# Kernel optimization log

Hardware: AMD Instinct MI355X
Metric: run time of the kernel (lower is better)

The kernel has to match this reference:

```python
import jax, jax.numpy as jnp
import numpy as np

NODE_CARDS = [119, 5, 12, 12, 10, 6, 6, 2, 2]
EDGE_CARDS = [5, 6, 2]
HIDDEN = 256
LAYERS = 5
N = 60000
E = 180000
G = 2048  # num graphs (fixed num_segments)
BN_EPS = 1e-5

_NODE_OFFS = np.concatenate([[0], np.cumsum(NODE_CARDS[:-1])]).astype(np.int32)
_EDGE_OFFS = np.concatenate([[0], np.cumsum(EDGE_CARDS[:-1])]).astype(np.int32)
_NODE_MAX = np.asarray(NODE_CARDS, np.int32) - 1
_EDGE_MAX = np.asarray(EDGE_CARDS, np.int32) - 1


def _cat_sum(x, table, maxs, offs):
    # x: [N, F] int; table: [sum(cards), H] -> [N, H]
    idx = jnp.clip(x, 0, maxs[None, :]) + offs[None, :]
    return table[idx].sum(axis=1)


def setup_inputs() -> dict:
    key = jax.random.key(0)
    ks = jax.random.split(key, 32)
    w = 0.0625  # ~ xavier for 256

    def nrm(k, shape, s=w):
        return jax.random.normal(k, shape, dtype=jnp.float32) * s

    inp = {
        'x': jax.random.randint(ks[0], (N, len(NODE_CARDS)), 0, 119, dtype=jnp.int32),
        'edge_index': jax.random.randint(ks[1], (2, E), 0, N, dtype=jnp.int32),
        'edge_attr': jax.random.randint(ks[2], (E, len(EDGE_CARDS)), 0, 6, dtype=jnp.int32),
        'batch': jnp.sort(jax.random.randint(ks[3], (N,), 0, G, dtype=jnp.int32)),
        # embeddings
        'node_emb': nrm(ks[4], (int(sum(NODE_CARDS)), HIDDEN), 0.1),
        'edge_emb': nrm(ks[5], (int(sum(EDGE_CARDS)), HIDDEN), 0.1),
        'vn_emb': nrm(ks[6], (1, HIDDEN), 0.1),
        # GINE conv: eps + 2-layer MLP per layer (stacked)
        'eps': jnp.zeros((LAYERS,), jnp.float32),
        'W1': nrm(ks[7], (LAYERS, HIDDEN, HIDDEN)),
        'b1': jnp.zeros((LAYERS, HIDDEN), jnp.float32),
        'W2': nrm(ks[8], (LAYERS, HIDDEN, HIDDEN)),
        'b2': jnp.zeros((LAYERS, HIDDEN), jnp.float32),
        # BatchNorm (eval mode: running stats)
        'bn_gamma': jnp.ones((LAYERS, HIDDEN), jnp.float32),
        'bn_beta': jnp.zeros((LAYERS, HIDDEN), jnp.float32),
        'bn_mean': nrm(ks[9], (LAYERS, HIDDEN), 0.02),
        'bn_var': jnp.ones((LAYERS, HIDDEN), jnp.float32),
        # virtual-node MLP per layer
        'vW1': nrm(ks[10], (LAYERS, HIDDEN, HIDDEN)),
        'vb1': jnp.zeros((LAYERS, HIDDEN), jnp.float32),
        'vW2': nrm(ks[11], (LAYERS, HIDDEN, HIDDEN)),
        'vb2': jnp.zeros((LAYERS, HIDDEN), jnp.float32),
        # head MLP (2 layers: hidden->hidden->1)
        'hW1': nrm(ks[12], (HIDDEN, HIDDEN)),
        'hb1': jnp.zeros((HIDDEN,), jnp.float32),
        'hW2': nrm(ks[13], (HIDDEN, 1)),
        'hb2': jnp.zeros((1,), jnp.float32),
    }
    return inp


def reference(x, edge_index, edge_attr, batch,
              node_emb, edge_emb, vn_emb, eps,
              W1, b1, W2, b2,
              bn_gamma, bn_beta, bn_mean, bn_var,
              vW1, vb1, vW2, vb2,
              hW1, hb1, hW2, hb2):
    node_maxs = jnp.asarray(_NODE_MAX)
    node_offs = jnp.asarray(_NODE_OFFS)
    edge_maxs = jnp.asarray(_EDGE_MAX)
    edge_offs = jnp.asarray(_EDGE_OFFS)

    h = _cat_sum(x, node_emb, node_maxs, node_offs)          # [N, H]
    ea = _cat_sum(edge_attr, edge_emb, edge_maxs, edge_offs)  # [E, H]
    src, dst = edge_index[0], edge_index[1]

    vn = jnp.broadcast_to(vn_emb[0], (G, HIDDEN))  # [G, H]

    def mean_pool(h_):
        s = jax.ops.segment_sum(h_, batch, num_segments=G)
        cnt = jax.ops.segment_sum(jnp.ones((h_.shape[0], 1), h_.dtype), batch, num_segments=G)
        return s / jnp.maximum(cnt, 1.0)

    for l in range(LAYERS):
        h = h + vn[batch]
        # GINEConv: msg = relu(x_src + edge_attr); agg scatter-add onto dst
        msg = jax.nn.relu(h[src] + ea)                        # [E, H]
        agg = jax.ops.segment_sum(msg, dst, num_segments=N)   # [N, H]
        z = (1.0 + eps[l]) * h + agg
        z = jax.nn.relu(z @ W1[l] + b1[l]) @ W2[l] + b2[l]
        # BatchNorm1d (eval, running stats)
        z = (z - bn_mean[l]) * (bn_gamma[l] / jnp.sqrt(bn_var[l] + BN_EPS)) + bn_beta[l]
        h = jax.nn.relu(z)
        # virtual-node update
        g = mean_pool(h)
        vn = vn + (jax.nn.relu(g @ vW1[l] + vb1[l]) @ vW2[l] + vb2[l])

    g = mean_pool(h)                                          # [G, H]
    logits = (jax.nn.relu(g @ hW1 + hb1) @ hW2 + hb2).reshape(-1)  # [G]
    return logits
```

## Files before the change

### kernel.cpp

```cpp
#include <hip/hip_runtime.h>

#define NN 60000
#define NE 180000
#define NG 2048
#define HD 256
#define NL 5
#define CAP 32

typedef unsigned short u16;
typedef unsigned int u32;
typedef __bf16 bf16x8 __attribute__((ext_vector_type(8)));
typedef float f32x4 __attribute__((ext_vector_type(4)));

__device__ __forceinline__ u16 f2bf(float f) {
    u32 u = __builtin_bit_cast(u32, f);
    u += 0x7FFFu + ((u >> 16) & 1u);
    return (u16)(u >> 16);
}
__device__ __forceinline__ float bf2f(u16 s) {
    return __builtin_bit_cast(float, (u32)s << 16);
}
__device__ __forceinline__ void gload_lds16(const void* g, void* l) {
    __builtin_amdgcn_global_load_lds(
        (const __attribute__((address_space(1))) unsigned int*)g,
        (__attribute__((address_space(3))) unsigned int*)l, 16, 0, 0);
}

__constant__ int NODE_OFF[9]  = {0, 119, 124, 136, 148, 158, 164, 170, 172};
__constant__ int NODE_MAXC[9] = {118, 4, 11, 11, 9, 5, 5, 1, 1};

__global__ __launch_bounds__(256) void k_prep_weights(
    const float* __restrict__ W1, const float* __restrict__ W2,
    const float* __restrict__ vW1, const float* __restrict__ vW2,
    const float* __restrict__ hW1, u16* __restrict__ Wt)
{
    int mat = blockIdx.x >> 8;
    int n = blockIdx.x & 255;
    int k = threadIdx.x;
    const float* src;
    if (mat < 5)       src = W1 + (size_t)mat * 65536;
    else if (mat < 10) src = W2 + (size_t)(mat - 5) * 65536;
    else if (mat < 15) src = vW1 + (size_t)(mat - 10) * 65536;
    else if (mat < 20) src = vW2 + (size_t)(mat - 15) * 65536;
    else               src = hW1;
    Wt[(size_t)mat * 65536 + n * 256 + k] = f2bf(src[k * 256 + n]);
}

__global__ __launch_bounds__(256) void k_comb(const float* __restrict__ eemb,
                                              u16* __restrict__ comb)
{
    int r = blockIdx.x;
    int c = threadIdx.x;
    int a0 = r / 12, a1 = (r % 12) / 2, a2 = r & 1;
    comb[r * 256 + c] = f2bf(eemb[(0 + a0) * 256 + c] + eemb[(5 + a1) * 256 + c] +
                             eemb[(11 + a2) * 256 + c]);
}

__global__ __launch_bounds__(256) void k_starts(const int* __restrict__ batch,
                                                int* __restrict__ starts)
{
    int g = blockIdx.x * 256 + threadIdx.x;
    if (g > NG) return;
    int lo = 0, hi = NN;
    while (lo < hi) {
        int mid = (lo + hi) >> 1;
        if (batch[mid] < g) lo = mid + 1; else hi = mid;
    }
    starts[g] = lo;
}

__global__ __launch_bounds__(256) void k_vn_init(const float* __restrict__ vn_emb,
                                                 float* __restrict__ vn,
                                                 u16* __restrict__ vnbf)
{
    int i = blockIdx.x * 256 + threadIdx.x;
    float v = vn_emb[i & 255];
    vn[i] = v;
    vnbf[i] = f2bf(v);
}

__global__ __launch_bounds__(256) void k_embed(const int* __restrict__ x,
                                               const float* __restrict__ node_emb,
                                               u16* __restrict__ hbf)
{
    int i = blockIdx.x * 4 + (threadIdx.x >> 6);
    if (i >= NN) return;
    int c = (threadIdx.x & 63) * 4;
    float4 s = make_float4(0.f, 0.f, 0.f, 0.f);
#pragma unroll
    for (int f = 0; f < 9; ++f) {
        int xv = x[i * 9 + f];
        xv = xv < 0 ? 0 : (xv > NODE_MAXC[f] ? NODE_MAXC[f] : xv);
        const float4 t = *(const float4*)&node_emb[(size_t)(NODE_OFF[f] + xv) * 256 + c];
        s.x += t.x; s.y += t.y; s.z += t.z; s.w += t.w;
    }
    ushort4 o;
    o.x = f2bf(s.x); o.y = f2bf(s.y); o.z = f2bf(s.z); o.w = f2bf(s.w);
    *(ushort4*)&hbf[(size_t)i * 256 + c] = o;
}

__global__ __launch_bounds__(256) void k_bucket(
    const int* __restrict__ src, const int* __restrict__ dst,
    const int* __restrict__ eattr, int* __restrict__ deg, u32* __restrict__ slots)
{
    int e = blockIdx.x * 256 + threadIdx.x;
    if (e >= NE) return;
    int a0 = eattr[e * 3 + 0]; a0 = a0 < 0 ? 0 : (a0 > 4 ? 4 : a0);
    int a1 = eattr[e * 3 + 1]; a1 = a1 < 0 ? 0 : (a1 > 5 ? 5 : a1);
    int a2 = eattr[e * 3 + 2]; a2 = a2 < 0 ? 0 : (a2 > 1 ? 1 : a2);
    u32 code = (u32)(a0 * 12 + a1 * 2 + a2);
    int d = dst[e];
    int p = atomicAdd(&deg[d], 1);
    if (p < CAP) slots[(size_t)d * CAP + p] = (u32)src[e] | (code << 17);
}

__global__ __launch_bounds__(256) void k_agg(
    const u16* __restrict__ hbf, const u16* __restrict__ vnbf,
    const int* __restrict__ batch, const u32* __restrict__ slots,
    const int* __restrict__ deg, const u16* __restrict__ comb,
    u16* __restrict__ Abf, const float* __restrict__ epsp)
{
    int d = blockIdx.x * 4 + (threadIdx.x >> 6);
    int lane = threadIdx.x & 63;
    int c = lane * 4;
    int nd = deg[d];
    nd = nd > CAP ? CAP : nd;

    const u32* sl = slots + (size_t)d * CAP;
    u32 sv_l = (lane < nd) ? sl[lane] : 0u;
    int b_l = (lane < nd) ? batch[sv_l & 0x1FFFFu] : 0;

    float4 acc = make_float4(0.f, 0.f, 0.f, 0.f);
    for (int p = 0; p < nd; ++p) {
        u32 sv = (u32)__shfl((int)sv_l, p);
        int b  = __shfl(b_l, p);
        int s  = (int)(sv & 0x1FFFFu);
        int code = (int)(sv >> 17);
        const ushort4 hv = *(const ushort4*)&hbf[(size_t)s * 256 + c];
        const ushort4 vv = *(const ushort4*)&vnbf[(size_t)b * 256 + c];
        const ushort4 tv = *(const ushort4*)&comb[(size_t)code * 256 + c];
        acc.x += fmaxf(bf2f(hv.x) + bf2f(vv.x) + bf2f(tv.x), 0.f);
        acc.y += fmaxf(bf2f(hv.y) + bf2f(vv.y) + bf2f(tv.y), 0.f);
        acc.z += fmaxf(bf2f(hv.z) + bf2f(vv.z) + bf2f(tv.z), 0.f);
        acc.w += fmaxf(bf2f(hv.w) + bf2f(vv.w) + bf2f(tv.w), 0.f);
    }

    int bd = batch[d];
    float ep = 1.0f + *epsp;
    const ushort4 hd = *(const ushort4*)&hbf[(size_t)d * 256 + c];
    const ushort4 vd = *(const ushort4*)&vnbf[(size_t)bd * 256 + c];
    ushort4 o;
    o.x = f2bf((bf2f(hd.x) + bf2f(vd.x)) * ep + acc.x);
    o.y = f2bf((bf2f(hd.y) + bf2f(vd.y)) * ep + acc.y);
    o.z = f2bf((bf2f(hd.z) + bf2f(vd.z)) * ep + acc.z);
    o.w = f2bf((bf2f(hd.w) + bf2f(vd.w)) * ep + acc.w);
    *(ushort4*)&Abf[(size_t)d * 256 + c] = o;
}

template <int EPI>
__global__ __launch_bounds__(512) void k_mlp(
    const u16* __restrict__ A, const u16* __restrict__ W1t, const u16* __restrict__ W2t,
    const float* __restrict__ b1, const float* __restrict__ b2,
    u16* __restrict__ hbf,
    const float* __restrict__ bng, const float* __restrict__ bnb,
    const float* __restrict__ bnm, const float* __restrict__ bnv,
    float* __restrict__ vn, u16* __restrict__ vnbf, int M)
{
    __shared__ __align__(16) u16 Al[64 * 64];
    __shared__ __align__(16) u16 Bl[256 * 64];
    __shared__ __align__(16) u16 Tl[64 * 256];
    const int m0 = blockIdx.x * 64;
    const int tid = threadIdx.x, lane = tid & 63, wid = tid >> 6;
    const int wm = (wid >> 2) * 32, wn = (wid & 3) * 64;
    const int cl = lane & 15, rg = lane >> 4;
    f32x4 acc[2][4] = {};

    for (int k0 = 0; k0 < 256; k0 += 64) {
        __syncthreads();
        {
            int row = tid >> 3, cch = tid & 7;
            int g = cch ^ (row & 7);
            gload_lds16((const char*)A + (size_t)(m0 + row) * 512 + (size_t)k0 * 2 + (g << 4),
                        (char*)Al + ((wid * 64) << 4));
        }
#pragma unroll
        for (int i = 0; i < 4; ++i) {
            int slot = i * 512 + tid;
            int row = slot >> 3, cch = slot & 7;
            int g = cch ^ (row & 7);
            gload_lds16((const char*)W1t + (size_t)row * 512 + (size_t)k0 * 2 + (g << 4),
                        (char*)Bl + ((i * 512 + wid * 64) << 4));
        }
        __syncthreads();
#pragma unroll
        for (int kw = 0; kw < 2; ++kw) {
            int q = kw * 4 + (lane >> 4);
            bf16x8 af[2], bfr[4];
#pragma unroll
            for (int t = 0; t < 2; ++t) {
                int ar = wm + t * 16 + cl;
                af[t] = __builtin_bit_cast(bf16x8,
                    *(const uint4*)((const char*)Al + (ar << 7) + ((q ^ (ar & 7)) << 4)));
            }
#pragma unroll
            for (int t = 0; t < 4; ++t) {
                int br = wn + t * 16 + cl;
                bfr[t] = __builtin_bit_cast(bf16x8,
                    *(const uint4*)((const char*)Bl + (br << 7) + ((q ^ (br & 7)) << 4)));
            }
#pragma unroll
            for (int i = 0; i < 2; ++i)
#pragma unroll
                for (int j = 0; j < 4; ++j)
                    acc[i][j] = __builtin_amdgcn_mfma_f32_16x16x32_bf16(af[i], bfr[j], acc[i][j], 0, 0, 0);
        }
    }

#pragma unroll
    for (int j = 0; j < 4; ++j) {
        int col = wn + j * 16 + cl;
        float bv = b1[col];
#pragma unroll
        for (int i = 0; i < 2; ++i) {
#pragma unroll
            for (int r = 0; r < 4; ++r) {
                int row = wm + i * 16 + rg * 4 + r;
                float v = fmaxf(acc[i][j][r] + bv, 0.f);
                int byte = (row << 9) + ((((col >> 3) ^ (row & 7))) << 4) + ((col & 7) << 1);
                *(u16*)((char*)Tl + byte) = f2bf(v);
            }
        }
    }
    __syncthreads();

    f32x4 acc2[2][4] = {};
    for (int k0 = 0; k0 < 256; k0 += 64) {
        if (k0) __syncthreads();
#pragma unroll
        for (int i = 0; i < 4; ++i) {
            int slot = i * 512 + tid;
            int row = slot >> 3, cch = slot & 7;
            int g = cch ^ (row & 7);
            gload_lds16((const char*)W2t + (size_t)row * 512 + (size_t)k0 * 2 + (g << 4),
                        (char*)Bl + ((i * 512 + wid * 64) << 4));
        }
        __syncthreads();
#pragma unroll
        for (int kw = 0; kw < 2; ++kw) {
            int q = kw * 4 + (lane >> 4);
            int qt = (k0 >> 3) + q;
            bf16x8 af[2], bfr[4];
#pragma unroll
            for (int t = 0; t < 2; ++t) {
                int ar = wm + t * 16 + cl;
                af[t] = __builtin_bit_cast(bf16x8,
                    *(const uint4*)((const char*)Tl + (ar << 9) + ((qt ^ (ar & 7)) << 4)));
            }
#pragma unroll
            for (int t = 0; t < 4; ++t) {
                int br = wn + t * 16 + cl;
                bfr[t] = __builtin_bit_cast(bf16x8,
                    *(const uint4*)((const char*)Bl + (br << 7) + ((q ^ (br & 7)) << 4)));
            }
#pragma unroll
            for (int i = 0; i < 2; ++i)
#pragma unroll
                for (int j = 0; j < 4; ++j)
                    acc2[i][j] = __builtin_amdgcn_mfma_f32_16x16x32_bf16(af[i], bfr[j], acc2[i][j], 0, 0, 0);
        }
    }

#pragma unroll
    for (int j = 0; j < 4; ++j) {
        int gn = wn + j * 16 + cl;
        float bv = b2[gn];
        float sc = 0.f, sh = 0.f;
        if constexpr (EPI == 0) {
            sc = bng[gn] * rsqrtf(bnv[gn] + 1e-5f);
            sh = bnb[gn] - bnm[gn] * sc;
        }
#pragma unroll
        for (int i = 0; i < 2; ++i) {
#pragma unroll
            for (int r = 0; r < 4; ++r) {
                int gm = m0 + wm + i * 16 + rg * 4 + r;
                if (gm >= M) continue;
                float v = acc2[i][j][r] + bv;
                if constexpr (EPI == 0) {
                    hbf[(size_t)gm * 256 + gn] = f2bf(fmaxf(v * sc + sh, 0.f));
                } else {
                    size_t idx = (size_t)gm * 256 + gn;
                    float nv = vn[idx] + v;
                    vn[idx] = nv;
                    vnbf[idx] = f2bf(nv);
                }
            }
        }
    }
}

__global__ __launch_bounds__(512) void k_headf(
    const u16* __restrict__ A, const u16* __restrict__ W1t,
    const float* __restrict__ b1, const float* __restrict__ hW2,
    const float* __restrict__ hb2, float* __restrict__ out)
{
    __shared__ __align__(16) u16 Al[64 * 64];
    __shared__ __align__(16) u16 Bl[256 * 64];
    __shared__ __align__(16) u16 Tl[64 * 256];
    const int m0 = blockIdx.x * 64;
    const int tid = threadIdx.x, lane = tid & 63, wid = tid >> 6;
    const int wm = (wid >> 2) * 32, wn = (wid & 3) * 64;
    const int cl = lane & 15, rg = lane >> 4;
    f32x4 acc[2][4] = {};

    for (int k0 = 0; k0 < 256; k0 += 64) {
        __syncthreads();
        {
            int row = tid >> 3, cch = tid & 7;
            int g = cch ^ (row & 7);
            gload_lds16((const char*)A + (size_t)(m0 + row) * 512 + (size_t)k0 * 2 + (g << 4),
                        (char*)Al + ((wid * 64) << 4));
        }
#pragma unroll
        for (int i = 0; i < 4; ++i) {
            int slot = i * 512 + tid;
            int row = slot >> 3, cch = slot & 7;
            int g = cch ^ (row & 7);
            gload_lds16((const char*)W1t + (size_t)row * 512 + (size_t)k0 * 2 + (g << 4),
                        (char*)Bl + ((i * 512 + wid * 64) << 4));
        }
        __syncthreads();
#pragma unroll
        for (int kw = 0; kw < 2; ++kw) {
            int q = kw * 4 + (lane >> 4);
            bf16x8 af[2], bfr[4];
#pragma unroll
            for (int t = 0; t < 2; ++t) {
                int ar = wm + t * 16 + cl;
                af[t] = __builtin_bit_cast(bf16x8,
                    *(const uint4*)((const char*)Al + (ar << 7) + ((q ^ (ar & 7)) << 4)));
            }
#pragma unroll
            for (int t = 0; t < 4; ++t) {
                int br = wn + t * 16 + cl;
                bfr[t] = __builtin_bit_cast(bf16x8,
                    *(const uint4*)((const char*)Bl + (br << 7) + ((q ^ (br & 7)) << 4)));
            }
#pragma unroll
            for (int i = 0; i < 2; ++i)
#pragma unroll
                for (int j = 0; j < 4; ++j)
                    acc[i][j] = __builtin_amdgcn_mfma_f32_16x16x32_bf16(af[i], bfr[j], acc[i][j], 0, 0, 0);
        }
    }
#pragma unroll
    for (int j = 0; j < 4; ++j) {
        int col = wn + j * 16 + cl;
        float bv = b1[col];
#pragma unroll
        for (int i = 0; i < 2; ++i) {
#pragma unroll
            for (int r = 0; r < 4; ++r) {
                int row = wm + i * 16 + rg * 4 + r;
                float v = fmaxf(acc[i][j][r] + bv, 0.f);
                int byte = (row << 9) + ((((col >> 3) ^ (row & 7))) << 4) + ((col & 7) << 1);
                *(u16*)((char*)Tl + byte) = f2bf(v);
            }
        }
    }
    __syncthreads();

    int row = tid >> 3, oct = tid & 7;
    float s = 0.f;
#pragma unroll
    for (int c = 0; c < 32; ++c) {
        int col = oct * 32 + c;
        int byte = (row << 9) + ((((col >> 3) ^ (row & 7))) << 4) + ((col & 7) << 1);
        s += bf2f(*(const u16*)((const char*)Tl + byte)) * hW2[col];
    }
    s += __shfl_down(s, 4);
    s += __shfl_down(s, 2);
    s += __shfl_down(s, 1);
    if (oct == 0) out[m0 + row] = s + hb2[0];
}

__global__ __launch_bounds__(256) void k_pool(const u16* __restrict__ hbf,
                                              const int* __restrict__ starts,
                                              u16* __restrict__ gbf)
{
    int g = blockIdx.x;
    int c = threadIdx.x;
    int s0 = starts[g], s1 = starts[g + 1];
    float sum = 0.f;
    for (int i = s0; i < s1; ++i) sum += bf2f(hbf[(size_t)i * 256 + c]);
    float cnt = (float)(s1 - s0);
    gbf[(size_t)g * 256 + c] = f2bf(sum / fmaxf(cnt, 1.0f));
}

extern "C" void kernel_launch(void* const* d_in, const int* in_sizes, int n_in,
                              void* d_out, int out_size, void* d_ws, size_t ws_size,
                              hipStream_t stream)
{
    const int*   x        = (const int*)d_in[0];
    const int*   ei       = (const int*)d_in[1];
    const int*   eattr    = (const int*)d_in[2];
    const int*   batch    = (const int*)d_in[3];
    const float* node_emb = (const float*)d_in[4];
    const float* edge_emb = (const float*)d_in[5];
    const float* vn_emb   = (const float*)d_in[6];
    const float* eps      = (const float*)d_in[7];
    const float* W1       = (const float*)d_in[8];
    const float* b1       = (const float*)d_in[9];
    const float* W2       = (const float*)d_in[10];
    const float* b2       = (const float*)d_in[11];
    const float* bng      = (const float*)d_in[12];
    const float* bnb      = (const float*)d_in[13];
    const float* bnm      = (const float*)d_in[14];
    const float* bnv      = (const float*)d_in[15];
    const float* vW1      = (const float*)d_in[16];
    const float* vb1      = (const float*)d_in[17];
    const float* vW2      = (const float*)d_in[18];
    const float* vb2      = (const float*)d_in[19];
    const float* hW1      = (const float*)d_in[20];
    const float* hb1      = (const float*)d_in[21];
    const float* hW2      = (const float*)d_in[22];
    const float* hb2      = (const float*)d_in[23];
    float* out = (float*)d_out;

    char* ws = (char*)d_ws;
    size_t off = 0;
    auto alloc = [&](size_t b) {
        char* p = ws + off;
        off = (off + b + 255) & ~(size_t)255;
        return p;
    };
    u16*   hbf  = (u16*)alloc((size_t)NN * 256 * 2);
    u16*   Abf  = (u16*)alloc((size_t)NN * 256 * 2);
    float* vn   = (float*)alloc((size_t)NG * 256 * 4);
    u16*   vnbf = (u16*)alloc((size_t)NG * 256 * 2);
    u16*   gbf  = (u16*)alloc((size_t)NG * 256 * 2);
    u16*   Wt   = (u16*)alloc((size_t)21 * 65536 * 2);
    int*   starts = (int*)alloc((size_t)(NG + 1) * 4);
    u16*   comb = (u16*)alloc((size_t)60 * 256 * 2);
    int*   deg  = (int*)alloc((size_t)NN * 4);
    u32*   slots = (u32*)alloc((size_t)NN * CAP * 4);

    const int* srcI = ei;
    const int* dstI = ei + NE;

    k_prep_weights<<<21 * 256, 256, 0, stream>>>(W1, W2, vW1, vW2, hW1, Wt);
    k_comb<<<60, 256, 0, stream>>>(edge_emb, comb);
    k_starts<<<(NG + 1 + 255) / 256, 256, 0, stream>>>(batch, starts);
    k_vn_init<<<NG, 256, 0, stream>>>(vn_emb, vn, vnbf);
    k_embed<<<NN / 4, 256, 0, stream>>>(x, node_emb, hbf);
    hipMemsetAsync(deg, 0, (size_t)NN * 4, stream);
    k_bucket<<<(NE + 255) / 256, 256, 0, stream>>>(srcI, dstI, eattr, deg, slots);

    const int GBIG = (NN + 63) / 64;
    const int GSM  = NG / 64;

    for (int l = 0; l < NL; ++l) {
        k_agg<<<NN / 4, 256, 0, stream>>>(hbf, vnbf, batch, slots, deg, comb, Abf, eps + l);
        k_mlp<0><<<GBIG, 512, 0, stream>>>(Abf,
                                           Wt + (size_t)(0 + l) * 65536,
                                           Wt + (size_t)(5 + l) * 65536,
                                           b1 + l * 256, b2 + l * 256, hbf,
                                           bng + l * 256, bnb + l * 256,
                                           bnm + l * 256, bnv + l * 256,
                                           nullptr, nullptr, NN);
        k_pool<<<NG, 256, 0, stream>>>(hbf, starts, gbf);
        k_mlp<1><<<GSM, 512, 0, stream>>>(gbf,
                                          Wt + (size_t)(10 + l) * 65536,
                                          Wt + (size_t)(15 + l) * 65536,
                                          vb1 + l * 256, vb2 + l * 256, nullptr,
                                          nullptr, nullptr, nullptr, nullptr,
                                          vn, vnbf, NG);
    }
    k_pool<<<NG, 256, 0, stream>>>(hbf, starts, gbf);
    k_headf<<<GSM, 512, 0, stream>>>(gbf, Wt + (size_t)20 * 65536, hb1, hW2, hb2, out);
}
```

Baseline: 620.2 us.

## Fuse aggregation, MLP, BN and pooling into one per-layer kernel

The neighbor aggregation is moved into the MLP kernel, so the aggregated rows are built directly in LDS and no longer round-trip through a global A buffer. Mean pooling becomes per-block segmented partial sums atomically added into an fp32 gsum buffer, which replaces the separate k_pool launches. The virtual-node MLP and the head now read gsum directly, and h is double-buffered because the fused kernel gathers neighbor rows from the previous layer while writing the next. The small init kernels are merged into one launch and the deg memset is folded into k_embed. In exchange, float atomics add nondeterministic summation order, and the gather latency is no longer overlapped with GEMM work from other blocks.

Result: faster. 601.8 us (-3.0%).

```diff
diff --git a/kernel.cpp b/kernel.cpp
--- a/kernel.cpp
+++ b/kernel.cpp
@@ -3,7 +3,6 @@
 #define NN 60000
 #define NE 180000
 #define NG 2048
-#define HD 256
 #define NL 5
 #define CAP 32
 
@@ -46,45 +45,44 @@
     Wt[(size_t)mat * 65536 + n * 256 + k] = f2bf(src[k * 256 + n]);
 }
 
-__global__ __launch_bounds__(256) void k_comb(const float* __restrict__ eemb,
-                                              u16* __restrict__ comb)
-{
-    int r = blockIdx.x;
-    int c = threadIdx.x;
-    int a0 = r / 12, a1 = (r % 12) / 2, a2 = r & 1;
-    comb[r * 256 + c] = f2bf(eemb[(0 + a0) * 256 + c] + eemb[(5 + a1) * 256 + c] +
-                             eemb[(11 + a2) * 256 + c]);
-}
-
-__global__ __launch_bounds__(256) void k_starts(const int* __restrict__ batch,
-                                                int* __restrict__ starts)
-{
-    int g = blockIdx.x * 256 + threadIdx.x;
-    if (g > NG) return;
-    int lo = 0, hi = NN;
-    while (lo < hi) {
-        int mid = (lo + hi) >> 1;
-        if (batch[mid] < g) lo = mid + 1; else hi = mid;
-    }
-    starts[g] = lo;
-}
-
-__global__ __launch_bounds__(256) void k_vn_init(const float* __restrict__ vn_emb,
-                                                 float* __restrict__ vn,
-                                                 u16* __restrict__ vnbf)
-{
-    int i = blockIdx.x * 256 + threadIdx.x;
-    float v = vn_emb[i & 255];
-    vn[i] = v;
-    vnbf[i] = f2bf(v);
+__global__ __launch_bounds__(256) void k_misc(
+    const float* __restrict__ eemb, const int* __restrict__ batch,
+    const float* __restrict__ vn_emb,
+    u16* __restrict__ comb, int* __restrict__ starts,
+    float* __restrict__ vn, u16* __restrict__ vnbf, float* __restrict__ gsum)
+{
+    int b = blockIdx.x;
+    if (b < 2048) {
+        int i = b * 256 + threadIdx.x;
+        float v = vn_emb[i & 255];
+        vn[i] = v;
+        vnbf[i] = f2bf(v);
+        gsum[i] = 0.f;
+    } else if (b < 2108) {
+        int r = b - 2048, c = threadIdx.x;
+        int a0 = r / 12, a1 = (r % 12) / 2, a2 = r & 1;
+        comb[r * 256 + c] = f2bf(eemb[a0 * 256 + c] + eemb[(5 + a1) * 256 + c] +
+                                 eemb[(11 + a2) * 256 + c]);
+    } else {
+        int g = (b - 2108) * 256 + threadIdx.x;
+        if (g > NG) return;
+        int lo = 0, hi = NN;
+        while (lo < hi) {
+            int mid = (lo + hi) >> 1;
+            if (batch[mid] < g) lo = mid + 1; else hi = mid;
+        }
+        starts[g] = lo;
+    }
 }
 
 __global__ __launch_bounds__(256) void k_embed(const int* __restrict__ x,
                                                const float* __restrict__ node_emb,
-                                               u16* __restrict__ hbf)
+                                               u16* __restrict__ hbf,
+                                               int* __restrict__ deg)
 {
     int i = blockIdx.x * 4 + (threadIdx.x >> 6);
     if (i >= NN) return;
+    if ((threadIdx.x & 63) == 0) deg[i] = 0;
     int c = (threadIdx.x & 63) * 4;
     float4 s = make_float4(0.f, 0.f, 0.f, 0.f);
 #pragma unroll
@@ -114,260 +112,278 @@
     if (p < CAP) slots[(size_t)d * CAP + p] = (u32)src[e] | (code << 17);
 }
 
-__global__ __launch_bounds__(256) void k_agg(
-    const u16* __restrict__ hbf, const u16* __restrict__ vnbf,
-    const int* __restrict__ batch, const u32* __restrict__ slots,
-    const int* __restrict__ deg, const u16* __restrict__ comb,
-    u16* __restrict__ Abf, const float* __restrict__ epsp)
-{
-    int d = blockIdx.x * 4 + (threadIdx.x >> 6);
-    int lane = threadIdx.x & 63;
-    int c = lane * 4;
-    int nd = deg[d];
-    nd = nd > CAP ? CAP : nd;
-
-    const u32* sl = slots + (size_t)d * CAP;
-    u32 sv_l = (lane < nd) ? sl[lane] : 0u;
-    int b_l = (lane < nd) ? batch[sv_l & 0x1FFFFu] : 0;
-
-    float4 acc = make_float4(0.f, 0.f, 0.f, 0.f);
-    for (int p = 0; p < nd; ++p) {
-        u32 sv = (u32)__shfl((int)sv_l, p);
-        int b  = __shfl(b_l, p);
-        int s  = (int)(sv & 0x1FFFFu);
-        int code = (int)(sv >> 17);
-        const ushort4 hv = *(const ushort4*)&hbf[(size_t)s * 256 + c];
-        const ushort4 vv = *(const ushort4*)&vnbf[(size_t)b * 256 + c];
-        const ushort4 tv = *(const ushort4*)&comb[(size_t)code * 256 + c];
-        acc.x += fmaxf(bf2f(hv.x) + bf2f(vv.x) + bf2f(tv.x), 0.f);
-        acc.y += fmaxf(bf2f(hv.y) + bf2f(vv.y) + bf2f(tv.y), 0.f);
-        acc.z += fmaxf(bf2f(hv.z) + bf2f(vv.z) + bf2f(tv.z), 0.f);
-        acc.w += fmaxf(bf2f(hv.w) + bf2f(vv.w) + bf2f(tv.w), 0.f);
-    }
-
-    int bd = batch[d];
-    float ep = 1.0f + *epsp;
-    const ushort4 hd = *(const ushort4*)&hbf[(size_t)d * 256 + c];
-    const ushort4 vd = *(const ushort4*)&vnbf[(size_t)bd * 256 + c];
-    ushort4 o;
-    o.x = f2bf((bf2f(hd.x) + bf2f(vd.x)) * ep + acc.x);
-    o.y = f2bf((bf2f(hd.y) + bf2f(vd.y)) * ep + acc.y);
-    o.z = f2bf((bf2f(hd.z) + bf2f(vd.z)) * ep + acc.z);
-    o.w = f2bf((bf2f(hd.w) + bf2f(vd.w)) * ep + acc.w);
-    *(ushort4*)&Abf[(size_t)d * 256 + c] = o;
-}
-
-template <int EPI>
-__global__ __launch_bounds__(512) void k_mlp(
-    const u16* __restrict__ A, const u16* __restrict__ W1t, const u16* __restrict__ W2t,
+__device__ __forceinline__ void stageW(const u16* __restrict__ W, u16* Bl,
+                                       int k0, int tid, int wid)
+{
+#pragma unroll
+    for (int i = 0; i < 4; ++i) {
+        int slot = i * 512 + tid;
+        int row = slot >> 3, cch = slot & 7;
+        int g = cch ^ (row & 7);
+        gload_lds16((const char*)W + (size_t)row * 512 + (size_t)k0 * 2 + (g << 4),
+                    (char*)Bl + ((i * 512 + wid * 64) << 4));
+    }
+}
+
+__device__ __forceinline__ void gemm64(const u16* Tl, u16* Bl, const u16* __restrict__ W,
+                                       f32x4 (&acc)[2][4], int wm, int wn,
+                                       int lane, int tid, int wid)
+{
+    const int cl = lane & 15;
+    for (int k0 = 0; k0 < 256; k0 += 64) {
+        __syncthreads();
+        stageW(W, Bl, k0, tid, wid);
+        __syncthreads();
+#pragma unroll
+        for (int kw = 0; kw < 2; ++kw) {
+            int q = kw * 4 + (lane >> 4);
+            int qt = (k0 >> 3) + q;
+            bf16x8 af[2], bfr[4];
+#pragma unroll
+            for (int t = 0; t < 2; ++t) {
+                int ar = wm + t * 16 + cl;
+                af[t] = __builtin_bit_cast(bf16x8,
+                    *(const uint4*)((const char*)Tl + (ar << 9) + ((qt ^ (ar & 7)) << 4)));
+            }
+#pragma unroll
+            for (int t = 0; t < 4; ++t) {
+                int br = wn + t * 16 + cl;
+                bfr[t] = __builtin_bit_cast(bf16x8,
+                    *(const uint4*)((const char*)Bl + (br << 7) + ((q ^ (br & 7)) << 4)));
+            }
+#pragma unroll
+            for (int i = 0; i < 2; ++i)
+#pragma unroll
+                for (int j = 0; j < 4; ++j)
+                    acc[i][j] = __builtin_amdgcn_mfma_f32_16x16x32_bf16(af[i], bfr[j], acc[i][j], 0, 0, 0);
+        }
+    }
+}
+
+__device__ __forceinline__ void writeT(u16* Tl, const f32x4 (&acc)[2][4],
+                                       const float* __restrict__ b1,
+                                       int wm, int wn, int lane)
+{
+    const int cl = lane & 15, rg = lane >> 4;
+#pragma unroll
+    for (int j = 0; j < 4; ++j) {
+        int col = wn + j * 16 + cl;
+        float bv = b1[col];
+#pragma unroll
+        for (int i = 0; i < 2; ++i)
+#pragma unroll
+            for (int r = 0; r < 4; ++r) {
+                int row = wm + i * 16 + rg * 4 + r;
+                float v = fmaxf(acc[i][j][r] + bv, 0.f);
+                *(u16*)((char*)Tl + (row << 9) + ((((col >> 3) ^ (row & 7))) << 4) +
+                        ((col & 7) << 1)) = f2bf(v);
+            }
+    }
+}
+
+__global__ __launch_bounds__(512) void k_mlpA(
+    const u16* __restrict__ hcur, u16* __restrict__ hnxt,
+    const u16* __restrict__ vnbf, const int* __restrict__ batch,
+    const u32* __restrict__ slots, const int* __restrict__ deg,
+    const u16* __restrict__ comb, const float* __restrict__ epsp,
+    const u16* __restrict__ W1t, const u16* __restrict__ W2t,
     const float* __restrict__ b1, const float* __restrict__ b2,
-    u16* __restrict__ hbf,
     const float* __restrict__ bng, const float* __restrict__ bnb,
     const float* __restrict__ bnm, const float* __restrict__ bnv,
-    float* __restrict__ vn, u16* __restrict__ vnbf, int M)
-{
-    __shared__ __align__(16) u16 Al[64 * 64];
+    float* __restrict__ gsum)
+{
+    __shared__ __align__(16) u16 Bl[256 * 64];
+    __shared__ __align__(16) u16 Tl[64 * 256];
+    __shared__ int batchLds[64];
+    const int m0 = blockIdx.x * 64;
+    const int tid = threadIdx.x, lane = tid & 63, wid = tid >> 6;
+    const int wm = (wid >> 2) * 32, wn = (wid & 3) * 64;
+    const int cl = lane & 15, rg = lane >> 4;
+
+    if (tid < 64) batchLds[tid] = (m0 + tid < NN) ? batch[m0 + tid] : -1;
+
+    {
+        const float ep = 1.0f + *epsp;
+        const int c = lane * 4;
+#pragma unroll
+        for (int n = 0; n < 8; ++n) {
+            int d = m0 + wid * 8 + n;
+            ushort4 o = make_ushort4(0, 0, 0, 0);
+            if (d < NN) {
+                int nd = deg[d]; nd = nd > CAP ? CAP : nd;
+                const u32* sl = slots + (size_t)d * CAP;
+                u32 sv_l = (lane < nd) ? sl[lane] : 0u;
+                int b_l = (lane < nd) ? batch[sv_l & 0x1FFFFu] : 0;
+                float4 acc = make_float4(0.f, 0.f, 0.f, 0.f);
+                for (int p = 0; p < nd; ++p) {
+                    u32 sv = (u32)__shfl((int)sv_l, p);
+                    int b  = __shfl(b_l, p);
+                    int s  = (int)(sv & 0x1FFFFu);
+                    int code = (int)(sv >> 17);
+                    const ushort4 hv = *(const ushort4*)&hcur[(size_t)s * 256 + c];
+                    const ushort4 vv = *(const ushort4*)&vnbf[(size_t)b * 256 + c];
+                    const ushort4 tv = *(const ushort4*)&comb[(size_t)code * 256 + c];
+                    acc.x += fmaxf(bf2f(hv.x) + bf2f(vv.x) + bf2f(tv.x), 0.f);
+                    acc.y += fmaxf(bf2f(hv.y) + bf2f(vv.y) + bf2f(tv.y), 0.f);
+                    acc.z += fmaxf(bf2f(hv.z) + bf2f(vv.z) + bf2f(tv.z), 0.f);
+                    acc.w += fmaxf(bf2f(hv.w) + bf2f(vv.w) + bf2f(tv.w), 0.f);
+                }
+                int bd = batch[d];
+                const ushort4 hd = *(const ushort4*)&hcur[(size_t)d * 256 + c];
+                const ushort4 vd = *(const ushort4*)&vnbf[(size_t)bd * 256 + c];
+                o.x = f2bf((bf2f(hd.x) + bf2f(vd.x)) * ep + acc.x);
+                o.y = f2bf((bf2f(hd.y) + bf2f(vd.y)) * ep + acc.y);
+                o.z = f2bf((bf2f(hd.z) + bf2f(vd.z)) * ep + acc.z);
+                o.w = f2bf((bf2f(hd.w) + bf2f(vd.w)) * ep + acc.w);
+            }
+            int row = wid * 8 + n;
+            *(ushort4*)((char*)Tl + (row << 9) + ((((c >> 3) ^ (row & 7))) << 4) +
+                        ((c & 7) << 1)) = o;
+        }
+    }
+    __syncthreads();
+
+    f32x4 acc1[2][4] = {};
+    gemm64(Tl, Bl, W1t, acc1, wm, wn, lane, tid, wid);
+    __syncthreads();
+    writeT(Tl, acc1, b1, wm, wn, lane);
+
+    f32x4 acc2[2][4] = {};
+    gemm64(Tl, Bl, W2t, acc2, wm, wn, lane, tid, wid);
+    __syncthreads();
+
+#pragma unroll
+    for (int j = 0; j < 4; ++j) {
+        int gn = wn + j * 16 + cl;
+        float bv = b2[gn];
+        float sc = bng[gn] * rsqrtf(bnv[gn] + 1e-5f);
+        float sh = bnb[gn] - bnm[gn] * sc;
+#pragma unroll
+        for (int i = 0; i < 2; ++i) {
+#pragma unroll
+            for (int r = 0; r < 4; ++r) {
+                int lr = wm + i * 16 + rg * 4 + r;
+                int gm = m0 + lr;
+                if (gm >= NN) continue;
+                float v = acc2[i][j][r] + bv;
+                u16 hb = f2bf(fmaxf(v * sc + sh, 0.f));
+                hnxt[(size_t)gm * 256 + gn] = hb;
+                Tl[lr * 256 + gn] = hb;
+            }
+        }
+    }
+    __syncthreads();
+
+    {
+        int col = tid & 255, half = tid >> 8;
+        float s = 0.f;
+        int gcur = -1;
+        int r0 = half * 32;
+        for (int r = r0; r < r0 + 32; ++r) {
+            int g = batchLds[r];
+            if (g < 0) break;
+            if (g != gcur) {
+                if (gcur >= 0) atomicAdd(&gsum[(size_t)gcur * 256 + col], s);
+                gcur = g; s = 0.f;
+            }
+            s += bf2f(Tl[r * 256 + col]);
+        }
+        if (gcur >= 0) atomicAdd(&gsum[(size_t)gcur * 256 + col], s);
+    }
+}
+
+__global__ __launch_bounds__(512) void k_vnmlp(
+    float* __restrict__ gsum, const int* __restrict__ starts,
+    const u16* __restrict__ W1t, const u16* __restrict__ W2t,
+    const float* __restrict__ b1, const float* __restrict__ b2,
+    float* __restrict__ vn, u16* __restrict__ vnbf)
+{
     __shared__ __align__(16) u16 Bl[256 * 64];
     __shared__ __align__(16) u16 Tl[64 * 256];
     const int m0 = blockIdx.x * 64;
     const int tid = threadIdx.x, lane = tid & 63, wid = tid >> 6;
     const int wm = (wid >> 2) * 32, wn = (wid & 3) * 64;
     const int cl = lane & 15, rg = lane >> 4;
-    f32x4 acc[2][4] = {};
-
-    for (int k0 = 0; k0 < 256; k0 += 64) {
-        __syncthreads();
-        {
-            int row = tid >> 3, cch = tid & 7;
-            int g = cch ^ (row & 7);
-            gload_lds16((const char*)A + (size_t)(m0 + row) * 512 + (size_t)k0 * 2 + (g << 4),
-                        (char*)Al + ((wid * 64) << 4));
-        }
-#pragma unroll
-        for (int i = 0; i < 4; ++i) {
-            int slot = i * 512 + tid;
-            int row = slot >> 3, cch = slot & 7;
-            int g = cch ^ (row & 7);
-            gload_lds16((const char*)W1t + (size_t)row * 512 + (size_t)k0 * 2 + (g << 4),
-                        (char*)Bl + ((i * 512 + wid * 64) << 4));
-        }
-        __syncthreads();
-#pragma unroll
-        for (int kw = 0; kw < 2; ++kw) {
-            int q = kw * 4 + (lane >> 4);
-            bf16x8 af[2], bfr[4];
-#pragma unroll
-            for (int t = 0; t < 2; ++t) {
-                int ar = wm + t * 16 + cl;
-                af[t] = __builtin_bit_cast(bf16x8,
-                    *(const uint4*)((const char*)Al + (ar << 7) + ((q ^ (ar & 7)) << 4)));
-            }
-#pragma unroll
-            for (int t = 0; t < 4; ++t) {
-                int br = wn + t * 16 + cl;
-                bfr[t] = __builtin_bit_cast(bf16x8,
-                    *(const uint4*)((const char*)Bl + (br << 7) + ((q ^ (br & 7)) << 4)));
-            }
-#pragma unroll
-            for (int i = 0; i < 2; ++i)
-#pragma unroll
-                for (int j = 0; j < 4; ++j)
-                    acc[i][j] = __builtin_amdgcn_mfma_f32_16x16x32_bf16(af[i], bfr[j], acc[i][j], 0, 0, 0);
-        }
-    }
-
-#pragma unroll
-    for (int j = 0; j < 4; ++j) {
-        int col = wn + j * 16 + cl;
-        float bv = b1[col];
-#pragma unroll
-        for (int i = 0; i < 2; ++i) {
-#pragma unroll
-            for (int r = 0; r < 4; ++r) {
-                int row = wm + i * 16 + rg * 4 + r;
-                float v = fmaxf(acc[i][j][r] + bv, 0.f);
-                int byte = (row << 9) + ((((col >> 3) ^ (row & 7))) << 4) + ((col & 7) << 1);
-                *(u16*)((char*)Tl + byte) = f2bf(v);
-            }
-        }
-    }
-    __syncthreads();
+
+    {
+        const int c = lane * 4;
+#pragma unroll
+        for (int n = 0; n < 8; ++n) {
+            int row = wid * 8 + n;
+            int g = m0 + row;
+            float4 sv = *(const float4*)&gsum[(size_t)g * 256 + c];
+            *(float4*)&gsum[(size_t)g * 256 + c] = make_float4(0.f, 0.f, 0.f, 0.f);
+            float cnt = (float)(starts[g + 1] - starts[g]);
+            float inv = 1.0f / fmaxf(cnt, 1.0f);
+            ushort4 o;
+            o.x = f2bf(sv.x * inv); o.y = f2bf(sv.y * inv);
+            o.z = f2bf(sv.z * inv); o.w = f2bf(sv.w * inv);
+            *(ushort4*)((char*)Tl + (row << 9) + ((((c >> 3) ^ (row & 7))) << 4) +
+                        ((c & 7) << 1)) = o;
+        }
+    }
+    __syncthreads();
+
+    f32x4 acc1[2][4] = {};
+    gemm64(Tl, Bl, W1t, acc1, wm, wn, lane, tid, wid);
+    __syncthreads();
+    writeT(Tl, acc1, b1, wm, wn, lane);
 
     f32x4 acc2[2][4] = {};
-    for (int k0 = 0; k0 < 256; k0 += 64) {
-        if (k0) __syncthreads();
-#pragma unroll
-        for (int i = 0; i < 4; ++i) {
-            int slot = i * 512 + tid;
-            int row = slot >> 3, cch = slot & 7;
-            int g = cch ^ (row & 7);
-            gload_lds16((const char*)W2t + (size_t)row * 512 + (size_t)k0 * 2 + (g << 4),
-                        (char*)Bl + ((i * 512 + wid * 64) << 4));
-        }
-        __syncthreads();
-#pragma unroll
-        for (int kw = 0; kw < 2; ++kw) {
-            int q = kw * 4 + (lane >> 4);
-            int qt = (k0 >> 3) + q;
-            bf16x8 af[2], bfr[4];
-#pragma unroll
-            for (int t = 0; t < 2; ++t) {
-                int ar = wm + t * 16 + cl;
-                af[t] = __builtin_bit_cast(bf16x8,
-                    *(const uint4*)((const char*)Tl + (ar << 9) + ((qt ^ (ar & 7)) << 4)));
-            }
-#pragma unroll
-            for (int t = 0; t < 4; ++t) {
-                int br = wn + t * 16 + cl;
-                bfr[t] = __builtin_bit_cast(bf16x8,
-                    *(const uint4*)((const char*)Bl + (br << 7) + ((q ^ (br & 7)) << 4)));
-            }
-#pragma unroll
-            for (int i = 0; i < 2; ++i)
-#pragma unroll
-                for (int j = 0; j < 4; ++j)
-                    acc2[i][j] = __builtin_amdgcn_mfma_f32_16x16x32_bf16(af[i], bfr[j], acc2[i][j], 0, 0, 0);
-        }
-    }
+    gemm64(Tl, Bl, W2t, acc2, wm, wn, lane, tid, wid);
 
 #pragma unroll
     for (int j = 0; j < 4; ++j) {
         int gn = wn + j * 16 + cl;
         float bv = b2[gn];
-        float sc = 0.f, sh = 0.f;
-        if constexpr (EPI == 0) {
-            sc = bng[gn] * rsqrtf(bnv[gn] + 1e-5f);
-            sh = bnb[gn] - bnm[gn] * sc;
-        }
 #pragma unroll
         for (int i = 0; i < 2; ++i) {
 #pragma unroll
             for (int r = 0; r < 4; ++r) {
                 int gm = m0 + wm + i * 16 + rg * 4 + r;
-                if (gm >= M) continue;
-                float v = acc2[i][j][r] + bv;
-                if constexpr (EPI == 0) {
-                    hbf[(size_t)gm * 256 + gn] = f2bf(fmaxf(v * sc + sh, 0.f));
-                } else {
-                    size_t idx = (size_t)gm * 256 + gn;
-                    float nv = vn[idx] + v;
-                    vn[idx] = nv;
-                    vnbf[idx] = f2bf(nv);
-                }
+                size_t idx = (size_t)gm * 256 + gn;
+                float nv = vn[idx] + acc2[i][j][r] + bv;
+                vn[idx] = nv;
+                vnbf[idx] = f2bf(nv);
             }
         }
     }
 }
 
 __global__ __launch_bounds__(512) void k_headf(
-    const u16* __restrict__ A, const u16* __restrict__ W1t,
-    const float* __restrict__ b1, const float* __restrict__ hW2,
-    const float* __restrict__ hb2, float* __restrict__ out)
-{
-    __shared__ __align__(16) u16 Al[64 * 64];
+    const float* __restrict__ gsum, const int* __restrict__ starts,
+    const u16* __restrict__ W1t, const float* __restrict__ b1,
+    const float* __restrict__ hW2, const float* __restrict__ hb2,
+    float* __restrict__ out)
+{
     __shared__ __align__(16) u16 Bl[256 * 64];
     __shared__ __align__(16) u16 Tl[64 * 256];
     const int m0 = blockIdx.x * 64;
     const int tid = threadIdx.x, lane = tid & 63, wid = tid >> 6;
     const int wm = (wid >> 2) * 32, wn = (wid & 3) * 64;
-    const int cl = lane & 15, rg = lane >> 4;
-    f32x4 acc[2][4] = {};
-
-    for (int k0 = 0; k0 < 256; k0 += 64) {
-        __syncthreads();
-        {
-            int row = tid >> 3, cch = tid & 7;
-            int g = cch ^ (row & 7);
-            gload_lds16((const char*)A + (size_t)(m0 + row) * 512 + (size_t)k0 * 2 + (g << 4),
-                        (char*)Al + ((wid * 64) << 4));
-        }
-#pragma unroll
-        for (int i = 0; i < 4; ++i) {
-            int slot = i * 512 + tid;
-            int row = slot >> 3, cch = slot & 7;
-            int g = cch ^ (row & 7);
-            gload_lds16((const char*)W1t + (size_t)row * 512 + (size_t)k0 * 2 + (g << 4),
-                        (char*)Bl + ((i * 512 + wid * 64) << 4));
-        }
-        __syncthreads();
-#pragma unroll
-        for (int kw = 0; kw < 2; ++kw) {
-            int q = kw * 4 + (lane >> 4);
-            bf16x8 af[2], bfr[4];
-#pragma unroll
-            for (int t = 0; t < 2; ++t) {
-                int ar = wm + t * 16 + cl;
-                af[t] = __builtin_bit_cast(bf16x8,
-                    *(const uint4*)((const char*)Al + (ar << 7) + ((q ^ (ar & 7)) << 4)));
-            }
-#pragma unroll
-            for (int t = 0; t < 4; ++t) {
-                int br = wn + t * 16 + cl;
-                bfr[t] = __builtin_bit_cast(bf16x8,
-                    *(const uint4*)((const char*)Bl + (br << 7) + ((q ^ (br & 7)) << 4)));
-            }
-#pragma unroll
-            for (int i = 0; i < 2; ++i)
-#pragma unroll
-                for (int j = 0; j < 4; ++j)
-                    acc[i][j] = __builtin_amdgcn_mfma_f32_16x16x32_bf16(af[i], bfr[j], acc[i][j], 0, 0, 0);
-        }
-    }
-#pragma unroll
-    for (int j = 0; j < 4; ++j) {
-        int col = wn + j * 16 + cl;
-        float bv = b1[col];
-#pragma unroll
-        for (int i = 0; i < 2; ++i) {
-#pragma unroll
-            for (int r = 0; r < 4; ++r) {
-                int row = wm + i * 16 + rg * 4 + r;
-                float v = fmaxf(acc[i][j][r] + bv, 0.f);
-                int byte = (row << 9) + ((((col >> 3) ^ (row & 7))) << 4) + ((col & 7) << 1);
-                *(u16*)((char*)Tl + byte) = f2bf(v);
-            }
-        }
-    }
+
+    {
+        const int c = lane * 4;
+#pragma unroll
+        for (int n = 0; n < 8; ++n) {
+            int row = wid * 8 + n;
+            int g = m0 + row;
+            float4 sv = *(const float4*)&gsum[(size_t)g * 256 + c];
+            float cnt = (float)(starts[g + 1] - starts[g]);
+            float inv = 1.0f / fmaxf(cnt, 1.0f);
+            ushort4 o;
+            o.x = f2bf(sv.x * inv); o.y = f2bf(sv.y * inv);
+            o.z = f2bf(sv.z * inv); o.w = f2bf(sv.w * inv);
+            *(ushort4*)((char*)Tl + (row << 9) + ((((c >> 3) ^ (row & 7))) << 4) +
+                        ((c & 7) << 1)) = o;
+        }
+    }
+    __syncthreads();
+
+    f32x4 acc1[2][4] = {};
+    gemm64(Tl, Bl, W1t, acc1, wm, wn, lane, tid, wid);
+    __syncthreads();
+    writeT(Tl, acc1, b1, wm, wn, lane);
     __syncthreads();
 
     int row = tid >> 3, oct = tid & 7;
@@ -382,19 +398,6 @@
     s += __shfl_down(s, 2);
     s += __shfl_down(s, 1);
     if (oct == 0) out[m0 + row] = s + hb2[0];
-}
-
-__global__ __launch_bounds__(256) void k_pool(const u16* __restrict__ hbf,
-                                              const int* __restrict__ starts,
-                                              u16* __restrict__ gbf)
-{
-    int g = blockIdx.x;
-    int c = threadIdx.x;
-    int s0 = starts[g], s1 = starts[g + 1];
-    float sum = 0.f;
-    for (int i = s0; i < s1; ++i) sum += bf2f(hbf[(size_t)i * 256 + c]);
-    float cnt = (float)(s1 - s0);
-    gbf[(size_t)g * 256 + c] = f2bf(sum / fmaxf(cnt, 1.0f));
 }
 
 extern "C" void kernel_launch(void* const* d_in, const int* in_sizes, int n_in,
@@ -434,11 +437,11 @@
         off = (off + b + 255) & ~(size_t)255;
         return p;
     };
-    u16*   hbf  = (u16*)alloc((size_t)NN * 256 * 2);
-    u16*   Abf  = (u16*)alloc((size_t)NN * 256 * 2);
+    u16*   hbf0 = (u16*)alloc((size_t)NN * 256 * 2);
+    u16*   hbf1 = (u16*)alloc((size_t)NN * 256 * 2);
     float* vn   = (float*)alloc((size_t)NG * 256 * 4);
     u16*   vnbf = (u16*)alloc((size_t)NG * 256 * 2);
-    u16*   gbf  = (u16*)alloc((size_t)NG * 256 * 2);
+    float* gsum = (float*)alloc((size_t)NG * 256 * 4);
     u16*   Wt   = (u16*)alloc((size_t)21 * 65536 * 2);
     int*   starts = (int*)alloc((size_t)(NG + 1) * 4);
     u16*   comb = (u16*)alloc((size_t)60 * 256 * 2);
@@ -449,33 +452,33 @@
     const int* dstI = ei + NE;
 
     k_prep_weights<<<21 * 256, 256, 0, stream>>>(W1, W2, vW1, vW2, hW1, Wt);
-    k_comb<<<60, 256, 0, stream>>>(edge_emb, comb);
-    k_starts<<<(NG + 1 + 255) / 256, 256, 0, stream>>>(batch, starts);
-    k_vn_init<<<NG, 256, 0, stream>>>(vn_emb, vn, vnbf);
-    k_embed<<<NN / 4, 256, 0, stream>>>(x, node_emb, hbf);
-    hipMemsetAsync(deg, 0, (size_t)NN * 4, stream);
+    k_misc<<<2117, 256, 0, stream>>>(edge_emb, batch, vn_emb, comb, starts, vn, vnbf, gsum);
+    k_embed<<<NN / 4, 256, 0, stream>>>(x, node_emb, hbf0, deg);
     k_bucket<<<(NE + 255) / 256, 256, 0, stream>>>(srcI, dstI, eattr, deg, slots);
 
     const int GBIG = (NN + 63) / 64;
     const int GSM  = NG / 64;
 
+    u16* hcur = hbf0;
+    u16* hnxt = hbf1;
     for (int l = 0; l < NL; ++l) {
-        k_agg<<<NN / 4, 256, 0, stream>>>(hbf, vnbf, batch, slots, deg, comb, Abf, eps + l);
-        k_mlp<0><<<GBIG, 512, 0, stream>>>(Abf,
-                                           Wt + (size_t)(0 + l) * 65536,
-                                           Wt + (size_t)(5 + l) * 65536,
-                                           b1 + l * 256, b2 + l * 256, hbf,
-                                           bng + l * 256, bnb + l * 256,
-                                           bnm + l * 256, bnv + l * 256,
-                                           nullptr, nullptr, NN);
-        k_pool<<<NG, 256, 0, stream>>>(hbf, starts, gbf);
-        k_mlp<1><<<GSM, 512, 0, stream>>>(gbf,
-                                          Wt + (size_t)(10 + l) * 65536,
-                                          Wt + (size_t)(15 + l) * 65536,
-                                          vb1 + l * 256, vb2 + l * 256, nullptr,
-                                          nullptr, nullptr, nullptr, nullptr,
-                                          vn, vnbf, NG);
-    }
-    k_pool<<<NG, 256, 0, stream>>>(hbf, starts, gbf);
-    k_headf<<<GSM, 512, 0, stream>>>(gbf, Wt + (size_t)20 * 65536, hb1, hW2, hb2, out);
-}
+        k_mlpA<<<GBIG, 512, 0, stream>>>(hcur, hnxt, vnbf, batch, slots, deg, comb,
+                                         eps + l,
+                                         Wt + (size_t)(0 + l) * 65536,
+                                         Wt + (size_t)(5 + l) * 65536,
+                                         b1 + l * 256, b2 + l * 256,
+                                         bng + l * 256, bnb + l * 256,
+                                         bnm + l * 256, bnv + l * 256,
+                                         gsum);
+        if (l < NL - 1) {
+            k_vnmlp<<<GSM, 512, 0, stream>>>(gsum, starts,
+                                             Wt + (size_t)(10 + l) * 65536,
+                                             Wt + (size_t)(15 + l) * 65536,
+                                             vb1 + l * 256, vb2 + l * 256,
+                                             vn, vnbf);
+        }
+        u16* t = hcur; hcur = hnxt; hnxt = t;
+    }
+    k_headf<<<GSM, 512, 0, stream>>>(gsum, starts, Wt + (size_t)20 * 65536,
+                                     hb1, hW2, hb2, out);
+}
```
